# Performance work log

Measured on AMD Instinct MI355X. Metric: run time of the kernel, lower is better.

Reference implementation:

```python
import jax, jax.numpy as jnp
import numpy as np

NUM_HEADS = 12
HEAD_DIM = 32
GP_NUM = 20


def setup_inputs() -> dict:
    key = jax.random.key(0)
    k1, k2, k3, k4 = jax.random.split(key, 4)
    B, H, W, C = 4, 32, 32, 384
    att = NUM_HEADS * HEAD_DIM  # == C (required by single group_mode)
    x = jax.random.normal(k1, (B, H, W, C), dtype=jnp.float32)
    W_qkv = jax.random.normal(k2, (3 * att, C), dtype=jnp.float32) * (C ** -0.5)
    W_proj = jax.random.normal(k3, (C, att), dtype=jnp.float32) * (att ** -0.5)
    W_gp = jax.random.normal(k4, (GP_NUM, C), dtype=jnp.float32) * (C ** -0.5)
    return {"x": x, "W_qkv": W_qkv, "W_proj": W_proj, "W_gp": W_gp}


def reference(x, W_qkv, W_proj, W_gp):
    B, H, W_, C = x.shape
    N = H * W_
    h, d = NUM_HEADS, HEAD_DIM
    scale = d ** -0.5

    qkv = x.reshape(B, N, C) @ W_qkv.T                      # [B,N,3hd]
    q, k, v = jnp.split(qkv, 3, axis=-1)
    q = q.reshape(B, N, h, d).transpose(0, 2, 1, 3)          # [B,h,N,d]
    k = k.reshape(B, N, h, d).transpose(0, 2, 1, 3)
    v = v.reshape(B, N, h, d).transpose(0, 2, 1, 3)

    attn = jax.nn.softmax(jnp.einsum('bhnd,bhmd->bhnm', q, k) * scale, axis=-1)

    # single group mode: hard top-1 group assignment from all-head q
    q_all = q.transpose(0, 2, 1, 3).reshape(B, N, h * d)     # [B,N,hd]
    gw = q_all @ W_gp.T                                      # [B,N,GP_NUM]
    oh = jax.nn.one_hot(jnp.argmax(gw, axis=-1), GP_NUM, dtype=attn.dtype)
    G = jnp.einsum('bng,bmg->bnm', oh, oh)                   # [B,N,N] same-group mask
    Gh = jnp.concatenate([
        jnp.broadcast_to(G[:, None], (B, h // 2, N, N)),
        jnp.broadcast_to(1.0 - G[:, None], (B, h // 2, N, N)),
    ], axis=1)                                               # [B,h,N,N]

    attn = attn * Gh
    # unusual column-wise renorm: sum over query axis (dim=2)
    attn = attn / (attn.sum(axis=2, keepdims=True) + 1e-8)

    out = jnp.einsum('bhnm,bhmd->bhnd', attn, v)
    out = out.transpose(0, 2, 1, 3).reshape(B, H, W_, h * d)
    return out @ W_proj.T
```

## Files before the change

kernel.cpp:

```cpp
#include <hip/hip_runtime.h>
#include <hip/hip_bf16.h>


#define B_    4
#define N_    1024
#define C_    384
#define H3_   1152
#define NH_   12
#define HD_   32
#define GP_   20
#define BH_   48
#define SCALE 0.17677669529663687f

typedef __attribute__((ext_vector_type(8))) short bf16x8;
typedef __attribute__((ext_vector_type(4))) float f32x4;

static __device__ __forceinline__ unsigned short f2bf(float x) {
  union { float f; unsigned u; } v; v.f = x;
  unsigned r = v.u + 0x7fff + ((v.u >> 16) & 1);
  return (unsigned short)(r >> 16);
}
static __device__ __forceinline__ float bf2f(unsigned short h) {
  union { unsigned u; float f; } v; v.u = ((unsigned)h) << 16;
  return v.f;
}

__global__ __launch_bounds__(256) void conv3(const float* __restrict__ x,
                                             const float* __restrict__ wq,
                                             const float* __restrict__ wp,
                                             unsigned short* __restrict__ xh,
                                             unsigned short* __restrict__ xl,
                                             unsigned short* __restrict__ wqh,
                                             unsigned short* __restrict__ wql,
                                             unsigned short* __restrict__ wph,
                                             unsigned short* __restrict__ wpl) {
  const int NX = (4096 * C_) / 4, NQ = (H3_ * C_) / 4, NP = (C_ * C_) / 4;
  int idx = blockIdx.x * 256 + threadIdx.x;
  const float* src; unsigned short *dh, *dl; int o;
  if (idx < NX)            { src = x;  dh = xh;  dl = xl;  o = idx; }
  else if (idx < NX + NQ)  { src = wq; dh = wqh; dl = wql; o = idx - NX; }
  else if (idx < NX + NQ + NP) { src = wp; dh = wph; dl = wpl; o = idx - NX - NQ; }
  else return;
  float4 v = *(const float4*)(src + (size_t)o * 4);
  float a[4] = {v.x, v.y, v.z, v.w};
  unsigned short h[4], lo[4];
  #pragma unroll
  for (int i = 0; i < 4; ++i) { h[i] = f2bf(a[i]); lo[i] = f2bf(a[i] - bf2f(h[i])); }
  uint2 ph = {(unsigned)h[0]  | ((unsigned)h[1]  << 16),
              (unsigned)h[2]  | ((unsigned)h[3]  << 16)};
  uint2 pl = {(unsigned)lo[0] | ((unsigned)lo[1] << 16),
              (unsigned)lo[2] | ((unsigned)lo[3] << 16)};
  *(uint2*)(dh + (size_t)o * 4) = ph;
  *(uint2*)(dl + (size_t)o * 4) = pl;
}

__global__ __launch_bounds__(256) void wgp_fuse(const float* __restrict__ Wqkv,
                                                const float* __restrict__ Wgp,
                                                double* __restrict__ M) {
  int idx = blockIdx.x * 256 + threadIdx.x;
  if (idx >= GP_ * C_) return;
  int g = idx / C_, c = idx % C_;
  double acc = 0.0;
  for (int j = 0; j < C_; ++j)
    acc += (double)Wgp[g * C_ + j] * (double)Wqkv[(size_t)j * C_ + c];
  M[idx] = acc;
}

__global__ __launch_bounds__(320) void group_assign2(const float* __restrict__ x,
                                                     const double* __restrict__ M,
                                                     int* __restrict__ group) {
  __shared__ double sc[16][GP_];
  int tid = threadIdx.x;
  int r = tid / GP_, g = tid % GP_;
  int n = blockIdx.x * 16 + r;
  const float* row = x + (size_t)n * C_;
  const double* w = M + (size_t)g * C_;
  double acc = 0.0;
  for (int c = 0; c < C_; ++c) acc += (double)row[c] * w[c];
  sc[r][g] = acc;
  __syncthreads();
  if (g == 0) {
    int best = 0; double bv = sc[r][0];
    #pragma unroll
    for (int j = 1; j < GP_; ++j)
      if (sc[r][j] > bv) { bv = sc[r][j]; best = j; }
    group[n] = best;
  }
}

__global__ __launch_bounds__(256) void gemm_qkv(
    const unsigned short* __restrict__ Ah_g, const unsigned short* __restrict__ Al_g,
    const unsigned short* __restrict__ Bh_g, const unsigned short* __restrict__ Bl_g,
    unsigned short* __restrict__ Qh, unsigned short* __restrict__ Ql,
    unsigned short* __restrict__ Kh, unsigned short* __restrict__ Kl,
    float* __restrict__ Vf) {
  __shared__ __align__(16) unsigned short sAh[2][128 * 32];
  __shared__ __align__(16) unsigned short sAl[2][128 * 32];
  __shared__ __align__(16) unsigned short sBh[2][64 * 32];
  __shared__ __align__(16) unsigned short sBl[2][64 * 32];
  int tid = threadIdx.x;
  int l = tid & 63, w = tid >> 6;
  int lanelo = l & 15, g16 = l >> 4;
  int wr = w >> 1, wc = w & 1;
  int flat = blockIdx.x;
  int swz = (flat & 7) * 72 + (flat >> 3);
  int bm = swz / 18, bn = swz % 18;

  int ra = tid >> 2, c4 = tid & 3;
  const unsigned short* gAh0 = Ah_g + (size_t)(bm * 128 + ra) * C_ + c4 * 8;
  const unsigned short* gAl0 = Al_g + (size_t)(bm * 128 + ra) * C_ + c4 * 8;
  const unsigned short* gBh0 = Bh_g + (size_t)(bn * 64 + ra) * C_ + c4 * 8;
  const unsigned short* gBl0 = Bl_g + (size_t)(bn * 64 + ra) * C_ + c4 * 8;
  int dsa = ra * 32 + ((c4 ^ (ra & 3)) * 8);

  uint4 r0 = *(const uint4*)(gAh0);
  uint4 r1 = *(const uint4*)(gAh0 + (size_t)64 * C_);
  uint4 r2 = *(const uint4*)(gAl0);
  uint4 r3 = *(const uint4*)(gAl0 + (size_t)64 * C_);
  uint4 r4 = *(const uint4*)(gBh0);
  uint4 r5 = *(const uint4*)(gBl0);

  f32x4 acc[4][2];
  #pragma unroll
  for (int i = 0; i < 4; ++i)
    #pragma unroll
    for (int j = 0; j < 2; ++j) acc[i][j] = (f32x4){0.f, 0.f, 0.f, 0.f};

  int p = 0;
  for (int kk = 0; kk < 12; ++kk) {
    *(uint4*)(&sAh[p][dsa])           = r0;
    *(uint4*)(&sAh[p][dsa + 64 * 32]) = r1;
    *(uint4*)(&sAl[p][dsa])           = r2;
    *(uint4*)(&sAl[p][dsa + 64 * 32]) = r3;
    *(uint4*)(&sBh[p][dsa])           = r4;
    *(uint4*)(&sBl[p][dsa])           = r5;
    __syncthreads();
    if (kk < 11) {
      int ko = (kk + 1) * 32;
      r0 = *(const uint4*)(gAh0 + ko);
      r1 = *(const uint4*)(gAh0 + (size_t)64 * C_ + ko);
      r2 = *(const uint4*)(gAl0 + ko);
      r3 = *(const uint4*)(gAl0 + (size_t)64 * C_ + ko);
      r4 = *(const uint4*)(gBh0 + ko);
      r5 = *(const uint4*)(gBl0 + ko);
    }
    bf16x8 ah[4], al[4], bh8[2], bl8[2];
    #pragma unroll
    for (int i = 0; i < 4; ++i) {
      int row = wr * 64 + i * 16 + lanelo;
      int off = row * 32 + ((g16 ^ (row & 3)) * 8);
      ah[i] = *(const bf16x8*)(&sAh[p][off]);
      al[i] = *(const bf16x8*)(&sAl[p][off]);
    }
    #pragma unroll
    for (int j = 0; j < 2; ++j) {
      int row = wc * 32 + j * 16 + lanelo;
      int off = row * 32 + ((g16 ^ (row & 3)) * 8);
      bh8[j] = *(const bf16x8*)(&sBh[p][off]);
      bl8[j] = *(const bf16x8*)(&sBl[p][off]);
    }
    #pragma unroll
    for (int i = 0; i < 4; ++i)
      #pragma unroll
      for (int j = 0; j < 2; ++j) {
        acc[i][j] = __builtin_amdgcn_mfma_f32_16x16x32_bf16(ah[i], bh8[j], acc[i][j], 0, 0, 0);
        acc[i][j] = __builtin_amdgcn_mfma_f32_16x16x32_bf16(ah[i], bl8[j], acc[i][j], 0, 0, 0);
        acc[i][j] = __builtin_amdgcn_mfma_f32_16x16x32_bf16(al[i], bh8[j], acc[i][j], 0, 0, 0);
      }
    p ^= 1;
  }

  int region = bn / 6;
  #pragma unroll
  for (int i = 0; i < 4; ++i) {
    int mm0 = bm * 128 + wr * 64 + i * 16 + g16 * 4;
    #pragma unroll
    for (int j = 0; j < 2; ++j) {
      int c = bn * 64 + wc * 32 + j * 16 + lanelo;
      int cc = c - region * 384;
      #pragma unroll
      for (int t = 0; t < 4; ++t) {
        int mm = mm0 + t;
        int b = mm >> 10, n = mm & 1023;
        float v = acc[i][j][t];
        if (region == 0) {
          v *= SCALE;
          unsigned short h = f2bf(v), lo = f2bf(v - bf2f(h));
          size_t idx = ((size_t)(b * NH_ + (cc >> 5)) * N_ + n) * HD_ + (cc & 31);
          Qh[idx] = h; Ql[idx] = lo;
        } else if (region == 1) {
          unsigned short h = f2bf(v), lo = f2bf(v - bf2f(h));
          size_t idx = ((size_t)(b * NH_ + (cc >> 5)) * N_ + n) * HD_ + (cc & 31);
          Kh[idx] = h; Kl[idx] = lo;
        } else {
          Vf[(size_t)mm * C_ + cc] = v;
        }
      }
    }
  }
}

__global__ __launch_bounds__(256) void gemm_proj(
    const unsigned short* __restrict__ Ah_g, const unsigned short* __restrict__ Al_g,
    const unsigned short* __restrict__ Bh_g, const unsigned short* __restrict__ Bl_g,
    float* __restrict__ Cm) {
  __shared__ __align__(16) unsigned short sAh[2][64 * 32];
  __shared__ __align__(16) unsigned short sAl[2][64 * 32];
  __shared__ __align__(16) unsigned short sBh[2][64 * 32];
  __shared__ __align__(16) unsigned short sBl[2][64 * 32];
  int tid = threadIdx.x;
  int l = tid & 63, w = tid >> 6;
  int lanelo = l & 15, g16 = l >> 4;
  int wr = w >> 1, wc = w & 1;
  int flat = blockIdx.x;
  int swz = (flat & 7) * 48 + (flat >> 3);
  int bm = swz / 6, bn = swz % 6;

  int ra = tid >> 2, c4 = tid & 3;
  const unsigned short* gAh0 = Ah_g + (size_t)(bm * 64 + ra) * C_ + c4 * 8;
  const unsigned short* gAl0 = Al_g + (size_t)(bm * 64 + ra) * C_ + c4 * 8;
  const unsigned short* gBh0 = Bh_g + (size_t)(bn * 64 + ra) * C_ + c4 * 8;
  const unsigned short* gBl0 = Bl_g + (size_t)(bn * 64 + ra) * C_ + c4 * 8;
  int dsa = ra * 32 + ((c4 ^ (ra & 3)) * 8);

  uint4 r0 = *(const uint4*)(gAh0);
  uint4 r1 = *(const uint4*)(gAl0);
  uint4 r2 = *(const uint4*)(gBh0);
  uint4 r3 = *(const uint4*)(gBl0);

  f32x4 acc[2][2];
  #pragma unroll
  for (int i = 0; i < 2; ++i)
    #pragma unroll
    for (int j = 0; j < 2; ++j) acc[i][j] = (f32x4){0.f, 0.f, 0.f, 0.f};

  int p = 0;
  for (int kk = 0; kk < 12; ++kk) {
    *(uint4*)(&sAh[p][dsa]) = r0;
    *(uint4*)(&sAl[p][dsa]) = r1;
    *(uint4*)(&sBh[p][dsa]) = r2;
    *(uint4*)(&sBl[p][dsa]) = r3;
    __syncthreads();
    if (kk < 11) {
      int ko = (kk + 1) * 32;
      r0 = *(const uint4*)(gAh0 + ko);
      r1 = *(const uint4*)(gAl0 + ko);
      r2 = *(const uint4*)(gBh0 + ko);
      r3 = *(const uint4*)(gBl0 + ko);
    }
    bf16x8 ah[2], al[2], bh8[2], bl8[2];
    #pragma unroll
    for (int i = 0; i < 2; ++i) {
      int row = wr * 32 + i * 16 + lanelo;
      int off = row * 32 + ((g16 ^ (row & 3)) * 8);
      ah[i] = *(const bf16x8*)(&sAh[p][off]);
      al[i] = *(const bf16x8*)(&sAl[p][off]);
    }
    #pragma unroll
    for (int j = 0; j < 2; ++j) {
      int row = wc * 32 + j * 16 + lanelo;
      int off = row * 32 + ((g16 ^ (row & 3)) * 8);
      bh8[j] = *(const bf16x8*)(&sBh[p][off]);
      bl8[j] = *(const bf16x8*)(&sBl[p][off]);
    }
    #pragma unroll
    for (int i = 0; i < 2; ++i)
      #pragma unroll
      for (int j = 0; j < 2; ++j) {
        acc[i][j] = __builtin_amdgcn_mfma_f32_16x16x32_bf16(ah[i], bh8[j], acc[i][j], 0, 0, 0);
        acc[i][j] = __builtin_amdgcn_mfma_f32_16x16x32_bf16(ah[i], bl8[j], acc[i][j], 0, 0, 0);
        acc[i][j] = __builtin_amdgcn_mfma_f32_16x16x32_bf16(al[i], bh8[j], acc[i][j], 0, 0, 0);
      }
    p ^= 1;
  }
  #pragma unroll
  for (int i = 0; i < 2; ++i) {
    int mm = bm * 64 + wr * 32 + i * 16 + g16 * 4;
    #pragma unroll
    for (int j = 0; j < 2; ++j) {
      int c = bn * 64 + wc * 32 + j * 16 + lanelo;
      #pragma unroll
      for (int t = 0; t < 4; ++t)
        Cm[(size_t)(mm + t) * C_ + c] = acc[i][j][t];
    }
  }
}

__global__ __launch_bounds__(256) void score3(const unsigned short* __restrict__ Qh,
                                              const unsigned short* __restrict__ Ql,
                                              const unsigned short* __restrict__ Kh,
                                              const unsigned short* __restrict__ Kl,
                                              const int* __restrict__ group,
                                              float* __restrict__ rinv,
                                              float* __restrict__ colpart) {
  __shared__ __align__(16) unsigned short kbufh[4096];
  __shared__ __align__(16) unsigned short kbufl[4096];
  __shared__ float colpart_s[4][1024];
  __shared__ int g_s[1024];
  int tid = threadIdx.x;
  int l = tid & 63, w = tid >> 6;
  int lanelo = l & 15, g16 = l >> 4;
  int flat = blockIdx.y * 16 + blockIdx.x;
  int nf = (flat & 7) * 96 + (flat >> 3);
  int bh = nf >> 4, blk = nf & 15;
  int b = bh / NH_;
  bool samehead = ((bh % NH_) < NH_ / 2);
  int q0 = blk * 64 + w * 16;
  size_t bhb = (size_t)bh * (N_ * HD_);

  *(int4*)&g_s[tid * 4] = *(const int4*)(group + b * N_ + tid * 4);
  bf16x8 aQh = *(const bf16x8*)(Qh + bhb + (size_t)(q0 + lanelo) * HD_ + g16 * 8);
  bf16x8 aQl = *(const bf16x8*)(Ql + bhb + (size_t)(q0 + lanelo) * HD_ + g16 * 8);
  __syncthreads();
  int gq[4];
  #pragma unroll
  for (int t = 0; t < 4; ++t) gq[t] = g_s[q0 + g16 * 4 + t];

  float s4[4] = {0.f, 0.f, 0.f, 0.f};
  for (int ch = 0; ch < 8; ++ch) {
    __syncthreads();
    #pragma unroll
    for (int t2 = 0; t2 < 2; ++t2) {
      int f2 = t2 * 256 + tid;
      int row = f2 >> 2, c4 = f2 & 3;
      uint4 vh = *(const uint4*)(Kh + bhb + (size_t)(ch * 128 + row) * HD_ + c4 * 8);
      uint4 vl = *(const uint4*)(Kl + bhb + (size_t)(ch * 128 + row) * HD_ + c4 * 8);
      int phys = row * 64 + ((c4 ^ (row & 3)) << 4);
      *(uint4*)((char*)kbufh + phys) = vh;
      *(uint4*)((char*)kbufl + phys) = vl;
    }
    __syncthreads();
    #pragma unroll
    for (int kt2 = 0; kt2 < 8; ++kt2) {
      int kvl = kt2 * 16 + lanelo;
      int phys = kvl * 64 + ((g16 ^ (kvl & 3)) << 4);
      bf16x8 bh8 = *(const bf16x8*)((char*)kbufh + phys);
      bf16x8 bl8 = *(const bf16x8*)((char*)kbufl + phys);
      f32x4 acc = {0.f, 0.f, 0.f, 0.f};
      acc = __builtin_amdgcn_mfma_f32_16x16x32_bf16(aQh, bh8, acc, 0, 0, 0);
      acc = __builtin_amdgcn_mfma_f32_16x16x32_bf16(aQh, bl8, acc, 0, 0, 0);
      acc = __builtin_amdgcn_mfma_f32_16x16x32_bf16(aQl, bh8, acc, 0, 0, 0);
      #pragma unroll
      for (int t = 0; t < 4; ++t) s4[t] += __expf(acc[t]);
    }
  }
  float ri[4];
  #pragma unroll
  for (int t = 0; t < 4; ++t) {
    #pragma unroll
    for (int off = 1; off < 16; off <<= 1) s4[t] += __shfl_xor(s4[t], off);
    ri[t] = 1.0f / s4[t];
  }
  if (lanelo == 0) {
    #pragma unroll
    for (int t = 0; t < 4; ++t)
      rinv[(size_t)bh * N_ + q0 + g16 * 4 + t] = ri[t];
  }

  for (int ch = 0; ch < 8; ++ch) {
    __syncthreads();
    #pragma unroll
    for (int t2 = 0; t2 < 2; ++t2) {
      int f2 = t2 * 256 + tid;
      int row = f2 >> 2, c4 = f2 & 3;
      uint4 vh = *(const uint4*)(Kh + bhb + (size_t)(ch * 128 + row) * HD_ + c4 * 8);
      uint4 vl = *(const uint4*)(Kl + bhb + (size_t)(ch * 128 + row) * HD_ + c4 * 8);
      int phys = row * 64 + ((c4 ^ (row & 3)) << 4);
      *(uint4*)((char*)kbufh + phys) = vh;
      *(uint4*)((char*)kbufl + phys) = vl;
    }
    __syncthreads();
    #pragma unroll
    for (int kt2 = 0; kt2 < 8; ++kt2) {
      int kt = ch * 8 + kt2;
      int kvl = kt2 * 16 + lanelo;
      int phys = kvl * 64 + ((g16 ^ (kvl & 3)) << 4);
      bf16x8 bh8 = *(const bf16x8*)((char*)kbufh + phys);
      bf16x8 bl8 = *(const bf16x8*)((char*)kbufl + phys);
      f32x4 acc = {0.f, 0.f, 0.f, 0.f};
      acc = __builtin_amdgcn_mfma_f32_16x16x32_bf16(aQh, bh8, acc, 0, 0, 0);
      acc = __builtin_amdgcn_mfma_f32_16x16x32_bf16(aQh, bl8, acc, 0, 0, 0);
      acc = __builtin_amdgcn_mfma_f32_16x16x32_bf16(aQl, bh8, acc, 0, 0, 0);
      int gcol = g_s[kt * 16 + lanelo];
      float cs = 0.f;
      #pragma unroll
      for (int t = 0; t < 4; ++t) {
        bool keep = ((gcol == gq[t]) == samehead);
        cs += keep ? __expf(acc[t]) * ri[t] : 0.f;
      }
      cs += __shfl_xor(cs, 16);
      cs += __shfl_xor(cs, 32);
      if (l < 16) colpart_s[w][kt * 16 + l] = cs;
    }
  }
  __syncthreads();
  int c0 = tid * 4;
  float4 p0 = *(float4*)&colpart_s[0][c0];
  float4 p1 = *(float4*)&colpart_s[1][c0];
  float4 p2 = *(float4*)&colpart_s[2][c0];
  float4 p3 = *(float4*)&colpart_s[3][c0];
  float4 rr = {p0.x + p1.x + p2.x + p3.x, p0.y + p1.y + p2.y + p3.y,
               p0.z + p1.z + p2.z + p3.z, p0.w + p1.w + p2.w + p3.w};
  *(float4*)(colpart + ((size_t)(bh * 16 + blk)) * 1024 + c0) = rr;
}

__global__ __launch_bounds__(256) void vsplit(const float* __restrict__ colpart,
                                              const float* __restrict__ Vf,
                                              unsigned short* __restrict__ Vth,
                                              unsigned short* __restrict__ Vtl) {
  __shared__ float red[256];
  __shared__ float colinv_s[16];
  __shared__ unsigned short vh_s[32][16];
  __shared__ unsigned short vl_s[32][16];
  int tid = threadIdx.x;
  int flat = blockIdx.y * 64 + blockIdx.x;
  int nf = (flat & 7) * 384 + (flat >> 3);
  int bh = nf >> 6, mt = nf & 63;
  int b = bh / NH_, hd = bh % NH_;

  int p = tid >> 4, m16 = tid & 15;
  red[tid] = colpart[((size_t)(bh * 16 + p)) * 1024 + mt * 16 + m16];
  __syncthreads();
  #pragma unroll
  for (int st = 128; st >= 16; st >>= 1) {
    if (tid < st) red[tid] += red[tid + st];
    __syncthreads();
  }
  if (tid < 16) colinv_s[tid] = 1.0f / (red[tid] + 1e-8f);
  __syncthreads();
  if (tid < 128) {
    int m = tid >> 3, d4 = (tid & 7) * 4;
    float4 v = *(const float4*)(Vf + ((size_t)(b * N_ + mt * 16 + m)) * C_ +
                                hd * HD_ + d4);
    float ci = colinv_s[m];
    float va[4] = {v.x * ci, v.y * ci, v.z * ci, v.w * ci};
    #pragma unroll
    for (int i = 0; i < 4; ++i) {
      unsigned short h = f2bf(va[i]);
      vh_s[d4 + i][m] = h;
      vl_s[d4 + i][m] = f2bf(va[i] - bf2f(h));
    }
  }
  __syncthreads();
  if (tid < 64) {
    int d = tid >> 1, m8 = (tid & 1) * 8;
    uint4 h = *(uint4*)&vh_s[d][m8];
    *(uint4*)(Vth + ((size_t)bh * HD_ + d) * N_ + mt * 16 + m8) = h;
  } else if (tid < 128) {
    int t2 = tid - 64;
    int d = t2 >> 1, m8 = (t2 & 1) * 8;
    uint4 lo = *(uint4*)&vl_s[d][m8];
    *(uint4*)(Vtl + ((size_t)bh * HD_ + d) * N_ + mt * 16 + m8) = lo;
  }
}

__global__ __launch_bounds__(256) void pv3(const unsigned short* __restrict__ Qh,
                                           const unsigned short* __restrict__ Ql,
                                           const unsigned short* __restrict__ Kh,
                                           const unsigned short* __restrict__ Kl,
                                           const unsigned short* __restrict__ Vth,
                                           const unsigned short* __restrict__ Vtl,
                                           const int* __restrict__ group,
                                           const float* __restrict__ rinv,
                                           unsigned short* __restrict__ aoh,
                                           unsigned short* __restrict__ aol) {
  __shared__ __align__(16) unsigned short kbufh[4096];
  __shared__ __align__(16) unsigned short kbufl[4096];
  __shared__ __align__(16) unsigned short vbufh[4096];
  __shared__ __align__(16) unsigned short vbufl[4096];
  __shared__ __align__(16) float bounce[4][512];
  __shared__ int g_s[1024];
  int tid = threadIdx.x;
  int l = tid & 63, w = tid >> 6;
  int lanelo = l & 15, g16 = l >> 4;
  int flat = blockIdx.y * 16 + blockIdx.x;
  int nf = (flat & 7) * 96 + (flat >> 3);
  int bh = nf >> 4, blk = nf & 15;
  int b = bh / NH_, hd = bh % NH_;
  bool samehead = (hd < NH_ / 2);
  int q0 = blk * 64 + w * 16;
  size_t bhb = (size_t)bh * (N_ * HD_);

  *(int4*)&g_s[tid * 4] = *(const int4*)(group + b * N_ + tid * 4);
  bf16x8 aQh = *(const bf16x8*)(Qh + bhb + (size_t)(q0 + lanelo) * HD_ + g16 * 8);
  bf16x8 aQl = *(const bf16x8*)(Ql + bhb + (size_t)(q0 + lanelo) * HD_ + g16 * 8);
  float ri[4];
  #pragma unroll
  for (int t = 0; t < 4; ++t)
    ri[t] = rinv[(size_t)bh * N_ + q0 + g16 * 4 + t];
  __syncthreads();
  int gq[4];
  #pragma unroll
  for (int t = 0; t < 4; ++t) gq[t] = g_s[q0 + g16 * 4 + t];

  f32x4 o0 = {0.f, 0.f, 0.f, 0.f};
  f32x4 o1 = {0.f, 0.f, 0.f, 0.f};

  for (int ch = 0; ch < 8; ++ch) {
    __syncthreads();
    #pragma unroll
    for (int t2 = 0; t2 < 2; ++t2) {
      int f2 = t2 * 256 + tid;
      int row = f2 >> 2, c4 = f2 & 3;
      uint4 vh = *(const uint4*)(Kh + bhb + (size_t)(ch * 128 + row) * HD_ + c4 * 8);
      uint4 vl = *(const uint4*)(Kl + bhb + (size_t)(ch * 128 + row) * HD_ + c4 * 8);
      int phys = row * 64 + ((c4 ^ (row & 3)) << 4);
      *(uint4*)((char*)kbufh + phys) = vh;
      *(uint4*)((char*)kbufl + phys) = vl;
    }
    #pragma unroll
    for (int t2 = 0; t2 < 2; ++t2) {
      int f2 = t2 * 256 + tid;
      int d = f2 >> 4, c = f2 & 15;
      uint4 vh = *(const uint4*)(Vth + bhb + (size_t)d * N_ + ch * 128 + c * 8);
      uint4 vl = *(const uint4*)(Vtl + bhb + (size_t)d * N_ + ch * 128 + c * 8);
      int physc = c ^ (d & 15);
      *(uint4*)(vbufh + d * 128 + physc * 8) = vh;
      *(uint4*)(vbufl + d * 128 + physc * 8) = vl;
    }
    __syncthreads();

    #pragma unroll
    for (int pair = 0; pair < 4; ++pair) {
      f32x4 sa[2];
      #pragma unroll
      for (int half = 0; half < 2; ++half) {
        int kvl = pair * 32 + half * 16 + lanelo;
        int phys = kvl * 64 + ((g16 ^ (kvl & 3)) << 4);
        bf16x8 bh8 = *(const bf16x8*)((char*)kbufh + phys);
        bf16x8 bl8 = *(const bf16x8*)((char*)kbufl + phys);
        f32x4 acc = {0.f, 0.f, 0.f, 0.f};
        acc = __builtin_amdgcn_mfma_f32_16x16x32_bf16(aQh, bh8, acc, 0, 0, 0);
        acc = __builtin_amdgcn_mfma_f32_16x16x32_bf16(aQh, bl8, acc, 0, 0, 0);
        acc = __builtin_amdgcn_mfma_f32_16x16x32_bf16(aQl, bh8, acc, 0, 0, 0);
        sa[half] = acc;
      }
      #pragma unroll
      for (int half = 0; half < 2; ++half) {
        int kvloc = pair * 32 + half * 16 + lanelo;
        int gcol = g_s[ch * 128 + kvloc];
        int kv = half * 16 + lanelo;
        int chunk = kv >> 2;
        #pragma unroll
        for (int t = 0; t < 4; ++t) {
          bool keep = ((gcol == gq[t]) == samehead);
          float p = keep ? __expf(sa[half][t]) : 0.f;
          int q = g16 * 4 + t;
          bounce[w][q * 32 + ((chunk ^ (q & 7)) << 2) + (kv & 3)] = p;
        }
      }
      float pf[8];
      int q2 = lanelo;
      int c0i = (2 * g16) ^ (q2 & 7), c1i = (2 * g16 + 1) ^ (q2 & 7);
      *(float4*)&pf[0] = *(float4*)&bounce[w][q2 * 32 + c0i * 4];
      *(float4*)&pf[4] = *(float4*)&bounce[w][q2 * 32 + c1i * 4];
      bf16x8 pa;
      #pragma unroll
      for (int j = 0; j < 8; ++j) pa[j] = (short)f2bf(pf[j]);
      int vchunk = pair * 4 + g16;
      int d0 = lanelo, d1 = 16 + lanelo;
      bf16x8 v0h = *(const bf16x8*)(vbufh + d0 * 128 + ((vchunk ^ (d0 & 15)) << 3));
      bf16x8 v0l = *(const bf16x8*)(vbufl + d0 * 128 + ((vchunk ^ (d0 & 15)) << 3));
      bf16x8 v1h = *(const bf16x8*)(vbufh + d1 * 128 + ((vchunk ^ (d1 & 15)) << 3));
      bf16x8 v1l = *(const bf16x8*)(vbufl + d1 * 128 + ((vchunk ^ (d1 & 15)) << 3));
      o0 = __builtin_amdgcn_mfma_f32_16x16x32_bf16(pa, v0h, o0, 0, 0, 0);
      o0 = __builtin_amdgcn_mfma_f32_16x16x32_bf16(pa, v0l, o0, 0, 0, 0);
      o1 = __builtin_amdgcn_mfma_f32_16x16x32_bf16(pa, v1h, o1, 0, 0, 0);
      o1 = __builtin_amdgcn_mfma_f32_16x16x32_bf16(pa, v1l, o1, 0, 0, 0);
    }
  }
  #pragma unroll
  for (int t = 0; t < 4; ++t) {
    size_t row = (size_t)(b * N_ + q0 + g16 * 4 + t) * C_ + hd * HD_;
    float v0 = o0[t] * ri[t], v1 = o1[t] * ri[t];
    unsigned short h;
    h = f2bf(v0); aoh[row + lanelo]      = h; aol[row + lanelo]      = f2bf(v0 - bf2f(h));
    h = f2bf(v1); aoh[row + 16 + lanelo] = h; aol[row + 16 + lanelo] = f2bf(v1 - bf2f(h));
  }
}

extern "C" void kernel_launch(void* const* d_in, const int* in_sizes, int n_in,
                              void* d_out, int out_size, void* d_ws, size_t ws_size,
                              hipStream_t stream) {
  const float* x     = (const float*)d_in[0];
  const float* Wqkv  = (const float*)d_in[1];
  const float* Wproj = (const float*)d_in[2];
  const float* Wgp   = (const float*)d_in[3];
  float* out = (float*)d_out;

  char* base = (char*)d_ws;
  size_t off = 0;
  auto alloc = [&](size_t bytes) {
    void* p = base + off;
    off += (bytes + 255) & ~(size_t)255;
    return p;
  };
  float*  Vf      = (float*)alloc(4096ull * C_ * 4);
  float*  rinv    = (float*)alloc((size_t)BH_ * N_ * 4);
  float*  colpart = (float*)alloc((size_t)BH_ * 16 * N_ * 4);
  double* Mgp     = (double*)alloc((size_t)GP_ * C_ * 8);
  int*    group   = (int*)alloc(4096ull * 4);
  unsigned short* xh  = (unsigned short*)alloc(4096ull * C_ * 2);
  unsigned short* xl  = (unsigned short*)alloc(4096ull * C_ * 2);
  unsigned short* Wqh = (unsigned short*)alloc((size_t)H3_ * C_ * 2);
  unsigned short* Wql = (unsigned short*)alloc((size_t)H3_ * C_ * 2);
  unsigned short* Wph = (unsigned short*)alloc((size_t)C_ * C_ * 2);
  unsigned short* Wpl = (unsigned short*)alloc((size_t)C_ * C_ * 2);
  unsigned short* aoh = (unsigned short*)alloc(4096ull * C_ * 2);
  unsigned short* aol = (unsigned short*)alloc(4096ull * C_ * 2);
  const size_t BSZ = (size_t)BH_ * N_ * HD_;
  unsigned short* Qh  = (unsigned short*)alloc(BSZ * 2);
  unsigned short* Ql  = (unsigned short*)alloc(BSZ * 2);
  unsigned short* Kh  = (unsigned short*)alloc(BSZ * 2);
  unsigned short* Kl  = (unsigned short*)alloc(BSZ * 2);
  unsigned short* Vth = (unsigned short*)alloc(BSZ * 2);
  unsigned short* Vtl = (unsigned short*)alloc(BSZ * 2);

  conv3<<<dim3(2112), 256, 0, stream>>>(x, Wqkv, Wproj, xh, xl, Wqh, Wql, Wph, Wpl);
  wgp_fuse<<<dim3(30), 256, 0, stream>>>(Wqkv, Wgp, Mgp);
  group_assign2<<<dim3(256), 320, 0, stream>>>(x, Mgp, group);
  gemm_qkv<<<dim3(576), 256, 0, stream>>>(xh, xl, Wqh, Wql,
                                          Qh, Ql, Kh, Kl, Vf);
  score3<<<dim3(16, BH_), 256, 0, stream>>>(Qh, Ql, Kh, Kl, group, rinv, colpart);
  vsplit<<<dim3(64, BH_), 256, 0, stream>>>(colpart, Vf, Vth, Vtl);
  pv3<<<dim3(16, BH_), 256, 0, stream>>>(Qh, Ql, Kh, Kl, Vth, Vtl, group,
                                         rinv, aoh, aol);
  gemm_proj<<<dim3(384), 256, 0, stream>>>(aoh, aol, Wph, Wpl, out);
}
```

Baseline: 167.2 us.

## Double query rows per wave in score/pv kernels, prefetch K/V into registers, use exp2

```diff
diff --git a/kernel.cpp b/kernel.cpp
--- a/kernel.cpp
+++ b/kernel.cpp
@@ -10,7 +10,7 @@
 #define HD_   32
 #define GP_   20
 #define BH_   48
-#define SCALE 0.17677669529663687f
+#define QSCALE 0.2550029971791444f
 
 typedef __attribute__((ext_vector_type(8))) short bf16x8;
 typedef __attribute__((ext_vector_type(4))) float f32x4;
@@ -184,7 +184,7 @@
         int b = mm >> 10, n = mm & 1023;
         float v = acc[i][j][t];
         if (region == 0) {
-          v *= SCALE;
+          v *= QSCALE;
           unsigned short h = f2bf(v), lo = f2bf(v - bf2f(h));
           size_t idx = ((size_t)(b * NH_ + (cc >> 5)) * N_ + n) * HD_ + (cc & 31);
           Qh[idx] = h; Ql[idx] = lo;
@@ -286,7 +286,7 @@
   }
 }
 
-__global__ __launch_bounds__(256) void score3(const unsigned short* __restrict__ Qh,
+__global__ __launch_bounds__(256) void score4(const unsigned short* __restrict__ Qh,
                                               const unsigned short* __restrict__ Ql,
                                               const unsigned short* __restrict__ Kh,
                                               const unsigned short* __restrict__ Kl,
@@ -300,97 +300,125 @@
   int tid = threadIdx.x;
   int l = tid & 63, w = tid >> 6;
   int lanelo = l & 15, g16 = l >> 4;
-  int flat = blockIdx.y * 16 + blockIdx.x;
-  int nf = (flat & 7) * 96 + (flat >> 3);
-  int bh = nf >> 4, blk = nf & 15;
+  int flat = blockIdx.y * 8 + blockIdx.x;
+  int nf = (flat & 7) * 48 + (flat >> 3);
+  int bh = nf >> 3, blk = nf & 7;
   int b = bh / NH_;
   bool samehead = ((bh % NH_) < NH_ / 2);
-  int q0 = blk * 64 + w * 16;
+  int q0 = blk * 128 + w * 32;
   size_t bhb = (size_t)bh * (N_ * HD_);
 
   *(int4*)&g_s[tid * 4] = *(const int4*)(group + b * N_ + tid * 4);
-  bf16x8 aQh = *(const bf16x8*)(Qh + bhb + (size_t)(q0 + lanelo) * HD_ + g16 * 8);
-  bf16x8 aQl = *(const bf16x8*)(Ql + bhb + (size_t)(q0 + lanelo) * HD_ + g16 * 8);
+  bf16x8 aQh[2], aQl[2];
+  #pragma unroll
+  for (int f = 0; f < 2; ++f) {
+    aQh[f] = *(const bf16x8*)(Qh + bhb + (size_t)(q0 + f * 16 + lanelo) * HD_ + g16 * 8);
+    aQl[f] = *(const bf16x8*)(Ql + bhb + (size_t)(q0 + f * 16 + lanelo) * HD_ + g16 * 8);
+  }
   __syncthreads();
-  int gq[4];
-  #pragma unroll
-  for (int t = 0; t < 4; ++t) gq[t] = g_s[q0 + g16 * 4 + t];
-
-  float s4[4] = {0.f, 0.f, 0.f, 0.f};
+  int gq[2][4];
+  #pragma unroll
+  for (int f = 0; f < 2; ++f)
+    #pragma unroll
+    for (int t = 0; t < 4; ++t) gq[f][t] = g_s[q0 + f * 16 + g16 * 4 + t];
+
+  int row0 = tid >> 2, c40 = tid & 3;
+  int row1 = (256 + tid) >> 2, c41 = tid & 3;
+  const unsigned short* kh0 = Kh + bhb + (size_t)row0 * HD_ + c40 * 8;
+  const unsigned short* kl0 = Kl + bhb + (size_t)row0 * HD_ + c40 * 8;
+  const unsigned short* kh1 = Kh + bhb + (size_t)row1 * HD_ + c41 * 8;
+  const unsigned short* kl1 = Kl + bhb + (size_t)row1 * HD_ + c41 * 8;
+  int ph0 = row0 * 64 + ((c40 ^ (row0 & 3)) << 4);
+  int ph1 = row1 * 64 + ((c41 ^ (row1 & 3)) << 4);
+
+  uint4 rh0 = *(const uint4*)(kh0), rh1 = *(const uint4*)(kh1);
+  uint4 rl0 = *(const uint4*)(kl0), rl1 = *(const uint4*)(kl1);
+
+  float s8[2][4] = {};
   for (int ch = 0; ch < 8; ++ch) {
+    if (ch) __syncthreads();
+    *(uint4*)((char*)kbufh + ph0) = rh0;
+    *(uint4*)((char*)kbufh + ph1) = rh1;
+    *(uint4*)((char*)kbufl + ph0) = rl0;
+    *(uint4*)((char*)kbufl + ph1) = rl1;
     __syncthreads();
-    #pragma unroll
-    for (int t2 = 0; t2 < 2; ++t2) {
-      int f2 = t2 * 256 + tid;
-      int row = f2 >> 2, c4 = f2 & 3;
-      uint4 vh = *(const uint4*)(Kh + bhb + (size_t)(ch * 128 + row) * HD_ + c4 * 8);
-      uint4 vl = *(const uint4*)(Kl + bhb + (size_t)(ch * 128 + row) * HD_ + c4 * 8);
-      int phys = row * 64 + ((c4 ^ (row & 3)) << 4);
-      *(uint4*)((char*)kbufh + phys) = vh;
-      *(uint4*)((char*)kbufl + phys) = vl;
-    }
-    __syncthreads();
+    if (ch < 7) {
+      int ko = (ch + 1) * 128 * HD_;
+      rh0 = *(const uint4*)(kh0 + ko); rh1 = *(const uint4*)(kh1 + ko);
+      rl0 = *(const uint4*)(kl0 + ko); rl1 = *(const uint4*)(kl1 + ko);
+    }
     #pragma unroll
     for (int kt2 = 0; kt2 < 8; ++kt2) {
       int kvl = kt2 * 16 + lanelo;
       int phys = kvl * 64 + ((g16 ^ (kvl & 3)) << 4);
       bf16x8 bh8 = *(const bf16x8*)((char*)kbufh + phys);
       bf16x8 bl8 = *(const bf16x8*)((char*)kbufl + phys);
-      f32x4 acc = {0.f, 0.f, 0.f, 0.f};
-      acc = __builtin_amdgcn_mfma_f32_16x16x32_bf16(aQh, bh8, acc, 0, 0, 0);
-      acc = __builtin_amdgcn_mfma_f32_16x16x32_bf16(aQh, bl8, acc, 0, 0, 0);
-      acc = __builtin_amdgcn_mfma_f32_16x16x32_bf16(aQl, bh8, acc, 0, 0, 0);
-      #pragma unroll
-      for (int t = 0; t < 4; ++t) s4[t] += __expf(acc[t]);
-    }
-  }
-  float ri[4];
-  #pragma unroll
-  for (int t = 0; t < 4; ++t) {
-    #pragma unroll
-    for (int off = 1; off < 16; off <<= 1) s4[t] += __shfl_xor(s4[t], off);
-    ri[t] = 1.0f / s4[t];
-  }
+      #pragma unroll
+      for (int f = 0; f < 2; ++f) {
+        f32x4 acc = {0.f, 0.f, 0.f, 0.f};
+        acc = __builtin_amdgcn_mfma_f32_16x16x32_bf16(aQh[f], bh8, acc, 0, 0, 0);
+        acc = __builtin_amdgcn_mfma_f32_16x16x32_bf16(aQh[f], bl8, acc, 0, 0, 0);
+        acc = __builtin_amdgcn_mfma_f32_16x16x32_bf16(aQl[f], bh8, acc, 0, 0, 0);
+        #pragma unroll
+        for (int t = 0; t < 4; ++t) s8[f][t] += exp2f(acc[t]);
+      }
+    }
+  }
+  float ri[2][4];
+  #pragma unroll
+  for (int f = 0; f < 2; ++f)
+    #pragma unroll
+    for (int t = 0; t < 4; ++t) {
+      float s = s8[f][t];
+      #pragma unroll
+      for (int off = 1; off < 16; off <<= 1) s += __shfl_xor(s, off);
+      ri[f][t] = 1.0f / s;
+    }
   if (lanelo == 0) {
     #pragma unroll
-    for (int t = 0; t < 4; ++t)
-      rinv[(size_t)bh * N_ + q0 + g16 * 4 + t] = ri[t];
-  }
-
+    for (int f = 0; f < 2; ++f)
+      #pragma unroll
+      for (int t = 0; t < 4; ++t)
+        rinv[(size_t)bh * N_ + q0 + f * 16 + g16 * 4 + t] = ri[f][t];
+  }
+
+  rh0 = *(const uint4*)(kh0); rh1 = *(const uint4*)(kh1);
+  rl0 = *(const uint4*)(kl0); rl1 = *(const uint4*)(kl1);
   for (int ch = 0; ch < 8; ++ch) {
     __syncthreads();
-    #pragma unroll
-    for (int t2 = 0; t2 < 2; ++t2) {
-      int f2 = t2 * 256 + tid;
-      int row = f2 >> 2, c4 = f2 & 3;
-      uint4 vh = *(const uint4*)(Kh + bhb + (size_t)(ch * 128 + row) * HD_ + c4 * 8);
-      uint4 vl = *(const uint4*)(Kl + bhb + (size_t)(ch * 128 + row) * HD_ + c4 * 8);
-      int phys = row * 64 + ((c4 ^ (row & 3)) << 4);
-      *(uint4*)((char*)kbufh + phys) = vh;
-      *(uint4*)((char*)kbufl + phys) = vl;
-    }
+    *(uint4*)((char*)kbufh + ph0) = rh0;
+    *(uint4*)((char*)kbufh + ph1) = rh1;
+    *(uint4*)((char*)kbufl + ph0) = rl0;
+    *(uint4*)((char*)kbufl + ph1) = rl1;
     __syncthreads();
+    if (ch < 7) {
+      int ko = (ch + 1) * 128 * HD_;
+      rh0 = *(const uint4*)(kh0 + ko); rh1 = *(const uint4*)(kh1 + ko);
+      rl0 = *(const uint4*)(kl0 + ko); rl1 = *(const uint4*)(kl1 + ko);
+    }
     #pragma unroll
     for (int kt2 = 0; kt2 < 8; ++kt2) {
-      int kt = ch * 8 + kt2;
       int kvl = kt2 * 16 + lanelo;
       int phys = kvl * 64 + ((g16 ^ (kvl & 3)) << 4);
       bf16x8 bh8 = *(const bf16x8*)((char*)kbufh + phys);
       bf16x8 bl8 = *(const bf16x8*)((char*)kbufl + phys);
-      f32x4 acc = {0.f, 0.f, 0.f, 0.f};
-      acc = __builtin_amdgcn_mfma_f32_16x16x32_bf16(aQh, bh8, acc, 0, 0, 0);
-      acc = __builtin_amdgcn_mfma_f32_16x16x32_bf16(aQh, bl8, acc, 0, 0, 0);
-      acc = __builtin_amdgcn_mfma_f32_16x16x32_bf16(aQl, bh8, acc, 0, 0, 0);
-      int gcol = g_s[kt * 16 + lanelo];
+      int gcol = g_s[ch * 128 + kvl];
       float cs = 0.f;
       #pragma unroll
-      for (int t = 0; t < 4; ++t) {
-        bool keep = ((gcol == gq[t]) == samehead);
-        cs += keep ? __expf(acc[t]) * ri[t] : 0.f;
+      for (int f = 0; f < 2; ++f) {
+        f32x4 acc = {0.f, 0.f, 0.f, 0.f};
+        acc = __builtin_amdgcn_mfma_f32_16x16x32_bf16(aQh[f], bh8, acc, 0, 0, 0);
+        acc = __builtin_amdgcn_mfma_f32_16x16x32_bf16(aQh[f], bl8, acc, 0, 0, 0);
+        acc = __builtin_amdgcn_mfma_f32_16x16x32_bf16(aQl[f], bh8, acc, 0, 0, 0);
+        #pragma unroll
+        for (int t = 0; t < 4; ++t) {
+          bool keep = ((gcol == gq[f][t]) == samehead);
+          cs += keep ? exp2f(acc[t]) * ri[f][t] : 0.f;
+        }
       }
       cs += __shfl_xor(cs, 16);
       cs += __shfl_xor(cs, 32);
-      if (l < 16) colpart_s[w][kt * 16 + l] = cs;
+      if (l < 16) colpart_s[w][ch * 128 + kt2 * 16 + l] = cs;
     }
   }
   __syncthreads();
@@ -401,7 +429,7 @@
   float4 p3 = *(float4*)&colpart_s[3][c0];
   float4 rr = {p0.x + p1.x + p2.x + p3.x, p0.y + p1.y + p2.y + p3.y,
                p0.z + p1.z + p2.z + p3.z, p0.w + p1.w + p2.w + p3.w};
-  *(float4*)(colpart + ((size_t)(bh * 16 + blk)) * 1024 + c0) = rr;
+  *(float4*)(colpart + ((size_t)(bh * 8 + blk)) * 1024 + c0) = rr;
 }
 
 __global__ __launch_bounds__(256) void vsplit(const float* __restrict__ colpart,
@@ -418,11 +446,12 @@
   int bh = nf >> 6, mt = nf & 63;
   int b = bh / NH_, hd = bh % NH_;
 
-  int p = tid >> 4, m16 = tid & 15;
-  red[tid] = colpart[((size_t)(bh * 16 + p)) * 1024 + mt * 16 + m16];
+  red[tid] = (tid < 128)
+      ? colpart[((size_t)(bh * 8 + (tid >> 4))) * 1024 + mt * 16 + (tid & 15)]
+      : 0.f;
   __syncthreads();
   #pragma unroll
-  for (int st = 128; st >= 16; st >>= 1) {
+  for (int st = 64; st >= 16; st >>= 1) {
     if (tid < st) red[tid] += red[tid + st];
     __syncthreads();
   }
@@ -454,7 +483,7 @@
   }
 }
 
-__global__ __launch_bounds__(256) void pv3(const unsigned short* __restrict__ Qh,
+__global__ __launch_bounds__(256) void pv4(const unsigned short* __restrict__ Qh,
                                            const unsigned short* __restrict__ Ql,
                                            const unsigned short* __restrict__ Kh,
                                            const unsigned short* __restrict__ Kl,
@@ -468,72 +497,99 @@
   __shared__ __align__(16) unsigned short kbufl[4096];
   __shared__ __align__(16) unsigned short vbufh[4096];
   __shared__ __align__(16) unsigned short vbufl[4096];
-  __shared__ __align__(16) float bounce[4][512];
+  __shared__ __align__(16) float bounce[4][1024];
   __shared__ int g_s[1024];
   int tid = threadIdx.x;
   int l = tid & 63, w = tid >> 6;
   int lanelo = l & 15, g16 = l >> 4;
-  int flat = blockIdx.y * 16 + blockIdx.x;
-  int nf = (flat & 7) * 96 + (flat >> 3);
-  int bh = nf >> 4, blk = nf & 15;
+  int flat = blockIdx.y * 8 + blockIdx.x;
+  int nf = (flat & 7) * 48 + (flat >> 3);
+  int bh = nf >> 3, blk = nf & 7;
   int b = bh / NH_, hd = bh % NH_;
   bool samehead = (hd < NH_ / 2);
-  int q0 = blk * 64 + w * 16;
+  int q0 = blk * 128 + w * 32;
   size_t bhb = (size_t)bh * (N_ * HD_);
 
   *(int4*)&g_s[tid * 4] = *(const int4*)(group + b * N_ + tid * 4);
-  bf16x8 aQh = *(const bf16x8*)(Qh + bhb + (size_t)(q0 + lanelo) * HD_ + g16 * 8);
-  bf16x8 aQl = *(const bf16x8*)(Ql + bhb + (size_t)(q0 + lanelo) * HD_ + g16 * 8);
-  float ri[4];
-  #pragma unroll
-  for (int t = 0; t < 4; ++t)
-    ri[t] = rinv[(size_t)bh * N_ + q0 + g16 * 4 + t];
+  bf16x8 aQh[2], aQl[2];
+  float ri[2][4];
+  #pragma unroll
+  for (int f = 0; f < 2; ++f) {
+    aQh[f] = *(const bf16x8*)(Qh + bhb + (size_t)(q0 + f * 16 + lanelo) * HD_ + g16 * 8);
+    aQl[f] = *(const bf16x8*)(Ql + bhb + (size_t)(q0 + f * 16 + lanelo) * HD_ + g16 * 8);
+    #pragma unroll
+    for (int t = 0; t < 4; ++t)
+      ri[f][t] = rinv[(size_t)bh * N_ + q0 + f * 16 + g16 * 4 + t];
+  }
   __syncthreads();
-  int gq[4];
-  #pragma unroll
-  for (int t = 0; t < 4; ++t) gq[t] = g_s[q0 + g16 * 4 + t];
-
-  f32x4 o0 = {0.f, 0.f, 0.f, 0.f};
-  f32x4 o1 = {0.f, 0.f, 0.f, 0.f};
+  int gq[2][4];
+  #pragma unroll
+  for (int f = 0; f < 2; ++f)
+    #pragma unroll
+    for (int t = 0; t < 4; ++t) gq[f][t] = g_s[q0 + f * 16 + g16 * 4 + t];
+
+  int krow0 = tid >> 2, kc0 = tid & 3;
+  int krow1 = (256 + tid) >> 2;
+  const unsigned short* kh0 = Kh + bhb + (size_t)krow0 * HD_ + kc0 * 8;
+  const unsigned short* kl0 = Kl + bhb + (size_t)krow0 * HD_ + kc0 * 8;
+  const unsigned short* kh1 = Kh + bhb + (size_t)krow1 * HD_ + kc0 * 8;
+  const unsigned short* kl1 = Kl + bhb + (size_t)krow1 * HD_ + kc0 * 8;
+  int kp0 = krow0 * 64 + ((kc0 ^ (krow0 & 3)) << 4);
+  int kp1 = krow1 * 64 + ((kc0 ^ (krow1 & 3)) << 4);
+  int vd0 = tid >> 4, vc0 = tid & 15;
+  int vd1 = (256 + tid) >> 4;
+  const unsigned short* vh0 = Vth + bhb + (size_t)vd0 * N_ + vc0 * 8;
+  const unsigned short* vl0 = Vtl + bhb + (size_t)vd0 * N_ + vc0 * 8;
+  const unsigned short* vh1 = Vth + bhb + (size_t)vd1 * N_ + vc0 * 8;
+  const unsigned short* vl1 = Vtl + bhb + (size_t)vd1 * N_ + vc0 * 8;
+  int vp0 = vd0 * 128 + (vc0 ^ (vd0 & 15)) * 8;
+  int vp1 = vd1 * 128 + (vc0 ^ (vd1 & 15)) * 8;
+
+  uint4 krh0 = *(const uint4*)(kh0), krh1 = *(const uint4*)(kh1);
+  uint4 krl0 = *(const uint4*)(kl0), krl1 = *(const uint4*)(kl1);
+  uint4 vrh0 = *(const uint4*)(vh0), vrh1 = *(const uint4*)(vh1);
+  uint4 vrl0 = *(const uint4*)(vl0), vrl1 = *(const uint4*)(vl1);
+
+  f32x4 o00 = {0.f,0.f,0.f,0.f}, o01 = {0.f,0.f,0.f,0.f};
+  f32x4 o10 = {0.f,0.f,0.f,0.f}, o11 = {0.f,0.f,0.f,0.f};
 
   for (int ch = 0; ch < 8; ++ch) {
+    if (ch) __syncthreads();
+    *(uint4*)((char*)kbufh + kp0) = krh0;
+    *(uint4*)((char*)kbufh + kp1) = krh1;
+    *(uint4*)((char*)kbufl + kp0) = krl0;
+    *(uint4*)((char*)kbufl + kp1) = krl1;
+    *(uint4*)(vbufh + vp0) = vrh0;
+    *(uint4*)(vbufh + vp1) = vrh1;
+    *(uint4*)(vbufl + vp0) = vrl0;
+    *(uint4*)(vbufl + vp1) = vrl1;
     __syncthreads();
-    #pragma unroll
-    for (int t2 = 0; t2 < 2; ++t2) {
-      int f2 = t2 * 256 + tid;
-      int row = f2 >> 2, c4 = f2 & 3;
-      uint4 vh = *(const uint4*)(Kh + bhb + (size_t)(ch * 128 + row) * HD_ + c4 * 8);
-      uint4 vl = *(const uint4*)(Kl + bhb + (size_t)(ch * 128 + row) * HD_ + c4 * 8);
-      int phys = row * 64 + ((c4 ^ (row & 3)) << 4);
-      *(uint4*)((char*)kbufh + phys) = vh;
-      *(uint4*)((char*)kbufl + phys) = vl;
-    }
-    #pragma unroll
-    for (int t2 = 0; t2 < 2; ++t2) {
-      int f2 = t2 * 256 + tid;
-      int d = f2 >> 4, c = f2 & 15;
-      uint4 vh = *(const uint4*)(Vth + bhb + (size_t)d * N_ + ch * 128 + c * 8);
-      uint4 vl = *(const uint4*)(Vtl + bhb + (size_t)d * N_ + ch * 128 + c * 8);
-      int physc = c ^ (d & 15);
-      *(uint4*)(vbufh + d * 128 + physc * 8) = vh;
-      *(uint4*)(vbufl + d * 128 + physc * 8) = vl;
-    }
-    __syncthreads();
+    if (ch < 7) {
+      int kko = (ch + 1) * 128 * HD_;
+      int vko = (ch + 1) * 128;
+      krh0 = *(const uint4*)(kh0 + kko); krh1 = *(const uint4*)(kh1 + kko);
+      krl0 = *(const uint4*)(kl0 + kko); krl1 = *(const uint4*)(kl1 + kko);
+      vrh0 = *(const uint4*)(vh0 + vko); vrh1 = *(const uint4*)(vh1 + vko);
+      vrl0 = *(const uint4*)(vl0 + vko); vrl1 = *(const uint4*)(vl1 + vko);
+    }
 
     #pragma unroll
     for (int pair = 0; pair < 4; ++pair) {
-      f32x4 sa[2];
+      f32x4 sa[2][2];
       #pragma unroll
       for (int half = 0; half < 2; ++half) {
         int kvl = pair * 32 + half * 16 + lanelo;
         int phys = kvl * 64 + ((g16 ^ (kvl & 3)) << 4);
         bf16x8 bh8 = *(const bf16x8*)((char*)kbufh + phys);
         bf16x8 bl8 = *(const bf16x8*)((char*)kbufl + phys);
-        f32x4 acc = {0.f, 0.f, 0.f, 0.f};
-        acc = __builtin_amdgcn_mfma_f32_16x16x32_bf16(aQh, bh8, acc, 0, 0, 0);
-        acc = __builtin_amdgcn_mfma_f32_16x16x32_bf16(aQh, bl8, acc, 0, 0, 0);
-        acc = __builtin_amdgcn_mfma_f32_16x16x32_bf16(aQl, bh8, acc, 0, 0, 0);
-        sa[half] = acc;
+        #pragma unroll
+        for (int f = 0; f < 2; ++f) {
+          f32x4 acc = {0.f, 0.f, 0.f, 0.f};
+          acc = __builtin_amdgcn_mfma_f32_16x16x32_bf16(aQh[f], bh8, acc, 0, 0, 0);
+          acc = __builtin_amdgcn_mfma_f32_16x16x32_bf16(aQh[f], bl8, acc, 0, 0, 0);
+          acc = __builtin_amdgcn_mfma_f32_16x16x32_bf16(aQl[f], bh8, acc, 0, 0, 0);
+          sa[f][half] = acc;
+        }
       }
       #pragma unroll
       for (int half = 0; half < 2; ++half) {
@@ -542,40 +598,54 @@
         int kv = half * 16 + lanelo;
         int chunk = kv >> 2;
         #pragma unroll
-        for (int t = 0; t < 4; ++t) {
-          bool keep = ((gcol == gq[t]) == samehead);
-          float p = keep ? __expf(sa[half][t]) : 0.f;
-          int q = g16 * 4 + t;
-          bounce[w][q * 32 + ((chunk ^ (q & 7)) << 2) + (kv & 3)] = p;
-        }
-      }
-      float pf[8];
-      int q2 = lanelo;
-      int c0i = (2 * g16) ^ (q2 & 7), c1i = (2 * g16 + 1) ^ (q2 & 7);
-      *(float4*)&pf[0] = *(float4*)&bounce[w][q2 * 32 + c0i * 4];
-      *(float4*)&pf[4] = *(float4*)&bounce[w][q2 * 32 + c1i * 4];
-      bf16x8 pa;
-      #pragma unroll
-      for (int j = 0; j < 8; ++j) pa[j] = (short)f2bf(pf[j]);
+        for (int f = 0; f < 2; ++f)
+          #pragma unroll
+          for (int t = 0; t < 4; ++t) {
+            bool keep = ((gcol == gq[f][t]) == samehead);
+            float p = keep ? exp2f(sa[f][half][t]) : 0.f;
+            int q = f * 16 + g16 * 4 + t;
+            bounce[w][q * 32 + ((chunk ^ (q & 7)) << 2) + (kv & 3)] = p;
+          }
+      }
+      int c0i = (2 * g16) ^ (lanelo & 7), c1i = (2 * g16 + 1) ^ (lanelo & 7);
+      float pf0[8], pf1[8];
+      *(float4*)&pf0[0] = *(float4*)&bounce[w][lanelo * 32 + c0i * 4];
+      *(float4*)&pf0[4] = *(float4*)&bounce[w][lanelo * 32 + c1i * 4];
+      *(float4*)&pf1[0] = *(float4*)&bounce[w][(16 + lanelo) * 32 + c0i * 4];
+      *(float4*)&pf1[4] = *(float4*)&bounce[w][(16 + lanelo) * 32 + c1i * 4];
+      bf16x8 pa0, pa1;
+      #pragma unroll
+      for (int j = 0; j < 8; ++j) {
+        pa0[j] = (short)f2bf(pf0[j]);
+        pa1[j] = (short)f2bf(pf1[j]);
+      }
       int vchunk = pair * 4 + g16;
       int d0 = lanelo, d1 = 16 + lanelo;
       bf16x8 v0h = *(const bf16x8*)(vbufh + d0 * 128 + ((vchunk ^ (d0 & 15)) << 3));
       bf16x8 v0l = *(const bf16x8*)(vbufl + d0 * 128 + ((vchunk ^ (d0 & 15)) << 3));
       bf16x8 v1h = *(const bf16x8*)(vbufh + d1 * 128 + ((vchunk ^ (d1 & 15)) << 3));
       bf16x8 v1l = *(const bf16x8*)(vbufl + d1 * 128 + ((vchunk ^ (d1 & 15)) << 3));
-      o0 = __builtin_amdgcn_mfma_f32_16x16x32_bf16(pa, v0h, o0, 0, 0, 0);
-      o0 = __builtin_amdgcn_mfma_f32_16x16x32_bf16(pa, v0l, o0, 0, 0, 0);
-      o1 = __builtin_amdgcn_mfma_f32_16x16x32_bf16(pa, v1h, o1, 0, 0, 0);
-      o1 = __builtin_amdgcn_mfma_f32_16x16x32_bf16(pa, v1l, o1, 0, 0, 0);
+      o00 = __builtin_amdgcn_mfma_f32_16x16x32_bf16(pa0, v0h, o00, 0, 0, 0);
+      o00 = __builtin_amdgcn_mfma_f32_16x16x32_bf16(pa0, v0l, o00, 0, 0, 0);
+      o01 = __builtin_amdgcn_mfma_f32_16x16x32_bf16(pa0, v1h, o01, 0, 0, 0);
+      o01 = __builtin_amdgcn_mfma_f32_16x16x32_bf16(pa0, v1l, o01, 0, 0, 0);
+      o10 = __builtin_amdgcn_mfma_f32_16x16x32_bf16(pa1, v0h, o10, 0, 0, 0);
+      o10 = __builtin_amdgcn_mfma_f32_16x16x32_bf16(pa1, v0l, o10, 0, 0, 0);
+      o11 = __builtin_amdgcn_mfma_f32_16x16x32_bf16(pa1, v1h, o11, 0, 0, 0);
+      o11 = __builtin_amdgcn_mfma_f32_16x16x32_bf16(pa1, v1l, o11, 0, 0, 0);
     }
   }
   #pragma unroll
   for (int t = 0; t < 4; ++t) {
-    size_t row = (size_t)(b * N_ + q0 + g16 * 4 + t) * C_ + hd * HD_;
-    float v0 = o0[t] * ri[t], v1 = o1[t] * ri[t];
+    size_t row0 = (size_t)(b * N_ + q0 + g16 * 4 + t) * C_ + hd * HD_;
+    size_t row1 = (size_t)(b * N_ + q0 + 16 + g16 * 4 + t) * C_ + hd * HD_;
+    float v00 = o00[t] * ri[0][t], v01 = o01[t] * ri[0][t];
+    float v10 = o10[t] * ri[1][t], v11 = o11[t] * ri[1][t];
     unsigned short h;
-    h = f2bf(v0); aoh[row + lanelo]      = h; aol[row + lanelo]      = f2bf(v0 - bf2f(h));
-    h = f2bf(v1); aoh[row + 16 + lanelo] = h; aol[row + 16 + lanelo] = f2bf(v1 - bf2f(h));
+    h = f2bf(v00); aoh[row0 + lanelo]      = h; aol[row0 + lanelo]      = f2bf(v00 - bf2f(h));
+    h = f2bf(v01); aoh[row0 + 16 + lanelo] = h; aol[row0 + 16 + lanelo] = f2bf(v01 - bf2f(h));
+    h = f2bf(v10); aoh[row1 + lanelo]      = h; aol[row1 + lanelo]      = f2bf(v10 - bf2f(h));
+    h = f2bf(v11); aoh[row1 + 16 + lanelo] = h; aol[row1 + 16 + lanelo] = f2bf(v11 - bf2f(h));
   }
 }
 
@@ -597,7 +667,7 @@
   };
   float*  Vf      = (float*)alloc(4096ull * C_ * 4);
   float*  rinv    = (float*)alloc((size_t)BH_ * N_ * 4);
-  float*  colpart = (float*)alloc((size_t)BH_ * 16 * N_ * 4);
+  float*  colpart = (float*)alloc((size_t)BH_ * 8 * N_ * 4);
   double* Mgp     = (double*)alloc((size_t)GP_ * C_ * 8);
   int*    group   = (int*)alloc(4096ull * 4);
   unsigned short* xh  = (unsigned short*)alloc(4096ull * C_ * 2);
@@ -621,9 +691,9 @@
   group_assign2<<<dim3(256), 320, 0, stream>>>(x, Mgp, group);
   gemm_qkv<<<dim3(576), 256, 0, stream>>>(xh, xl, Wqh, Wql,
                                           Qh, Ql, Kh, Kl, Vf);
-  score3<<<dim3(16, BH_), 256, 0, stream>>>(Qh, Ql, Kh, Kl, group, rinv, colpart);
+  score4<<<dim3(8, BH_), 256, 0, stream>>>(Qh, Ql, Kh, Kl, group, rinv, colpart);
   vsplit<<<dim3(64, BH_), 256, 0, stream>>>(colpart, Vf, Vth, Vtl);
-  pv3<<<dim3(16, BH_), 256, 0, stream>>>(Qh, Ql, Kh, Kl, Vth, Vtl, group,
-                                         rinv, aoh, aol);
+  pv4<<<dim3(8, BH_), 256, 0, stream>>>(Qh, Ql, Kh, Kl, Vth, Vtl, group,
+                                        rinv, aoh, aol);
   gemm_proj<<<dim3(384), 256, 0, stream>>>(aoh, aol, Wph, Wpl, out);
 }
```

Result: slower. 194.7 us (+16.5%).
